# Kernel optimization log

Measured on AMD Instinct MI355X. Metric: run time of the kernel, lower is better.

Reference implementation:

```python
import jax, jax.numpy as jnp
import numpy as np

B, N, DIN, DMID, DOUT, E = 64, 5000, 64, 128, 32, 80000


def setup_inputs() -> dict:
    key = jax.random.key(0)
    ks = jax.random.split(key, 12)
    p = lambda k, shape: jax.random.normal(k, shape, jnp.float32) * 0.05
    return {
        "x": jax.random.normal(ks[0], (B, N, DIN), jnp.float32),
        "edge_index": jax.random.randint(ks[1], (2, E), 0, N),
        "prev_hidden_state": jax.random.normal(ks[2], (B, N, DMID), jnp.float32),
        # GCNConv weights/biases for gates z, r, h
        "Wg_z": p(ks[3], (DIN, DMID)), "bg_z": jnp.zeros((DMID,), jnp.float32),
        "Wg_r": p(ks[4], (DIN, DMID)), "bg_r": jnp.zeros((DMID,), jnp.float32),
        "Wg_h": p(ks[5], (DIN, DMID)), "bg_h": jnp.zeros((DMID,), jnp.float32),
        # gate Linear layers on concat([conv_out, H]) -> DMID
        "Wl_z": p(ks[6], (2 * DMID, DMID)), "bl_z": jnp.zeros((DMID,), jnp.float32),
        "Wl_r": p(ks[7], (2 * DMID, DMID)), "bl_r": jnp.zeros((DMID,), jnp.float32),
        "Wl_h": p(ks[8], (2 * DMID, DMID)), "bl_h": jnp.zeros((DMID,), jnp.float32),
        # final output Linear
        "W_out": p(ks[9], (DMID, DOUT)), "b_out": jnp.zeros((DOUT,), jnp.float32),
    }


def reference(x, edge_index, prev_hidden_state,
              Wg_z, bg_z, Wg_r, bg_r, Wg_h, bg_h,
              Wl_z, bl_z, Wl_r, bl_r, Wl_h, bl_h,
              W_out, b_out):
    # GCN symmetric normalization with self-loops (pyg gcn_norm, improved=False)
    row, col = edge_index[0], edge_index[1]
    loop = jnp.arange(N)
    src = jnp.concatenate([row, loop])          # [E+N]
    dst = jnp.concatenate([col, loop])          # [E+N]
    ew = jnp.ones((E + N,), x.dtype)
    deg = jnp.zeros((N,), x.dtype).at[dst].add(ew)
    dis = jnp.where(deg > 0, jax.lax.rsqrt(jnp.maximum(deg, 1e-12)), 0.0)
    norm = dis[src] * ew * dis[dst]             # [E+N]

    def gcn(w, b):
        xw = jnp.einsum('bnd,de->bne', x, w)            # [B,N,DMID]
        msg = xw[:, src, :] * norm[None, :, None]       # gather + weight
        out = jnp.zeros((B, N, w.shape[1]), x.dtype).at[:, dst, :].add(msg)
        return out + b

    H = prev_hidden_state
    Z = jax.nn.sigmoid(jnp.concatenate([gcn(Wg_z, bg_z), H], -1) @ Wl_z + bl_z)
    R = jax.nn.sigmoid(jnp.concatenate([gcn(Wg_r, bg_r), H], -1) @ Wl_r + bl_r)
    Ht = jnp.tanh(jnp.concatenate([gcn(Wg_h, bg_h), H * R], -1) @ Wl_h + bl_h)
    H_new = Z * H + (1.0 - Z) * Ht                      # [B,N,DMID]

    y = jnp.mean(H_new, axis=1)                         # MeanAggregation over nodes
    y = jax.nn.relu(y) @ W_out + b_out                  # [B,DOUT]
    return (y, H_new)
```

## Files before the change

### kernel.cpp

```cpp
#include <hip/hip_runtime.h>
#include <cmath>

namespace {

constexpr int B = 64, N = 5000, DIN = 64, DMID = 128, DOUT = 32, E = 80000;

typedef unsigned short u16;
typedef __attribute__((ext_vector_type(8))) short short8;
typedef __attribute__((ext_vector_type(4))) float floatx4;

#define MFMA16(a, b, c) __builtin_amdgcn_mfma_f32_16x16x32_bf16((a), (b), (c), 0, 0, 0)

__device__ __forceinline__ u16 f2bf(float f) {
  union { float f; unsigned u; } v; v.f = f;
  unsigned r = v.u + 0x7FFFu + ((v.u >> 16) & 1u);
  return (u16)(r >> 16);
}
__device__ __forceinline__ float bf2f(u16 s) {
  union { unsigned u; float f; } v; v.u = ((unsigned)s) << 16;
  return v.f;
}
__device__ __forceinline__ float sigmoid_fast(float x) {
  return __builtin_amdgcn_rcpf(1.f + __expf(-x));
}
__device__ __forceinline__ float tanh_fast(float x) {
  return fmaf(2.f, __builtin_amdgcn_rcpf(1.f + __expf(-2.f * x)), -1.f);
}


__global__ void zero_kernel(int* counts, int* fill, float* msum) {
  int i = blockIdx.x * 256 + threadIdx.x;
  if (i < N) { counts[i] = 0; fill[i] = 0; }
  if (i < B * DMID) msum[i] = 0.f;
}

__global__ void count_kernel(const int* __restrict__ ei, int* counts) {
  int e = blockIdx.x * 256 + threadIdx.x;
  if (e < E) atomicAdd(&counts[ei[E + e]], 1);
}

__global__ void scan_kernel(const int* __restrict__ counts, int* rowptr, float* dis) {
  __shared__ int sdata[1024];
  const int tid = threadIdx.x;
  constexpr int CH = (N + 1023) / 1024;
  int local[CH];
  int s = 0;
  for (int i = 0; i < CH; i++) {
    int idx = tid * CH + i;
    int c = (idx < N) ? counts[idx] : 0;
    local[i] = s;
    s += c;
  }
  sdata[tid] = s;
  __syncthreads();
  for (int off = 1; off < 1024; off <<= 1) {
    int v = (tid >= off) ? sdata[tid - off] : 0;
    __syncthreads();
    sdata[tid] += v;
    __syncthreads();
  }
  int prev = (tid > 0) ? sdata[tid - 1] : 0;
  for (int i = 0; i < CH; i++) {
    int idx = tid * CH + i;
    if (idx < N) {
      rowptr[idx] = prev + local[i];
      dis[idx] = rsqrtf((float)(counts[idx] + 1));
    }
  }
  if (tid == 1023) rowptr[N] = sdata[1023];
}

__global__ void fill_kernel(const int* __restrict__ ei, const int* __restrict__ rowptr,
                            const float* __restrict__ dis, int* fill,
                            int* csr_src, float* csr_w) {
  int e = blockIdx.x * 256 + threadIdx.x;
  if (e >= E) return;
  int r = ei[e], c = ei[E + e];
  int pos = rowptr[c] + atomicAdd(&fill[c], 1);
  csr_src[pos] = r;
  csr_w[pos] = dis[r] * dis[c];
}


__global__ void pack_kernel(const float* Wgz, const float* Wgr, const float* Wgh,
                            const float* Wlz, const float* Wlr, const float* Wlh,
                            const float* bgz, const float* bgr, const float* bgh,
                            const float* blz, const float* blr, const float* blh,
                            u16* wcB, u16* whB, float* bcAll) {
  int t = blockIdx.x * 256 + threadIdx.x;
  const float* Wg[3] = {Wgz, Wgr, Wgh};
  const float* Wl[3] = {Wlz, Wlr, Wlh};
  const float* bg[3] = {bgz, bgr, bgh};
  const float* bl[3] = {blz, blr, blh};
  if (t < 48 * 64) {
    int chunk = t >> 6, lane = t & 63;
    int q = lane >> 4, lm = lane & 15;
    int g = chunk >> 4, rem = chunk & 15, kt = rem >> 3, nt = rem & 7;
    int n = nt * 16 + lm;
#pragma unroll
    for (int jj = 0; jj < 8; jj++) {
      int k = kt * 32 + q * 8 + jj;
      float acc = 0.f;
      for (int j = 0; j < DMID; j++)
        acc = fmaf(Wg[g][k * DMID + j], Wl[g][j * DMID + n], acc);
      wcB[(size_t)(chunk * 64 + lane) * 8 + jj] = f2bf(acc);
    }
  } else if (t < 48 * 64 + 96 * 64) {
    int t2 = t - 48 * 64;
    int chunk = t2 >> 6, lane = t2 & 63;
    int q = lane >> 4, lm = lane & 15;
    int g = chunk >> 5, rem = chunk & 31, kt = rem >> 3, nt = rem & 7;
    int n = nt * 16 + lm;
#pragma unroll
    for (int jj = 0; jj < 8; jj++) {
      int k = kt * 32 + q * 8 + jj;
      whB[(size_t)t2 * 8 + jj] = f2bf(Wl[g][(DMID + k) * DMID + n]);
    }
  } else {
    int t3 = t - 48 * 64 - 96 * 64;
    if (t3 < 384) {
      int g = t3 >> 7, n = t3 & 127;
      float acc = bl[g][n];
      for (int j = 0; j < DMID; j++)
        acc = fmaf(bg[g][j], Wl[g][j * DMID + n], acc);
      bcAll[t3] = acc;
    }
  }
}


__global__ __launch_bounds__(256) void agg_kernel(
    const float* __restrict__ x, const int* __restrict__ rowptr,
    const int* __restrict__ csr_src, const float* __restrict__ csr_w,
    const float* __restrict__ dis, u16* __restrict__ xs) {
  const int sub = threadIdx.x >> 4;
  const int l16 = threadIdx.x & 15;
  const int unit = blockIdx.x * 16 + sub;
  const int b = unit / N;
  const int n = unit - b * N;
  const float* xb = x + (size_t)b * N * DIN;
  const float d = dis[n];
  float4 v = *(const float4*)(xb + (size_t)n * DIN + l16 * 4);
  const float sw = d * d;
  float ax = v.x * sw, ay = v.y * sw, az = v.z * sw, aw = v.w * sw;
  const int s1 = rowptr[n + 1];
  int p = rowptr[n];
  for (; p + 2 <= s1; p += 2) {
    int i0 = csr_src[p], i1 = csr_src[p + 1];
    float w0 = csr_w[p], w1 = csr_w[p + 1];
    float4 a0 = *(const float4*)(xb + (size_t)i0 * DIN + l16 * 4);
    float4 a1 = *(const float4*)(xb + (size_t)i1 * DIN + l16 * 4);
    ax = fmaf(a0.x, w0, ax); ay = fmaf(a0.y, w0, ay);
    az = fmaf(a0.z, w0, az); aw = fmaf(a0.w, w0, aw);
    ax = fmaf(a1.x, w1, ax); ay = fmaf(a1.y, w1, ay);
    az = fmaf(a1.z, w1, az); aw = fmaf(a1.w, w1, aw);
  }
  if (p < s1) {
    int i0 = csr_src[p];
    float w0 = csr_w[p];
    float4 a0 = *(const float4*)(xb + (size_t)i0 * DIN + l16 * 4);
    ax = fmaf(a0.x, w0, ax); ay = fmaf(a0.y, w0, ay);
    az = fmaf(a0.z, w0, az); aw = fmaf(a0.w, w0, aw);
  }
  uint2 o;
  o.x = (unsigned)f2bf(ax) | ((unsigned)f2bf(ay) << 16);
  o.y = (unsigned)f2bf(az) | ((unsigned)f2bf(aw) << 16);
  *(uint2*)(xs + (size_t)unit * DIN + l16 * 4) = o;
}


constexpr int SH = 136;
constexpr int SX = 72;

__global__ __launch_bounds__(256, 4) void fused_mfma(
    const u16* __restrict__ xs, const float* __restrict__ H,
    const u16* __restrict__ wcB, const u16* __restrict__ whB,
    const float* __restrict__ bcAll,
    float* __restrict__ hnew, float* __restrict__ msum) {
  __shared__ u16 H_s[64 * SH];
  __shared__ u16 XS_s[64 * SX];

  const int tid = threadIdx.x;
  const int b = blockIdx.y;
  const int n0 = blockIdx.x * 64;
  const int lane = tid & 63, w = tid >> 6;
  const int q = lane >> 4, lm = lane & 15;
  const int w16 = w * 16;

#pragma unroll
  for (int i = 0; i < 2; i++) {
    int idx = i * 256 + tid;
    int row = idx >> 3, seg = idx & 7;
    uint4 v = make_uint4(0u, 0u, 0u, 0u);
    if (n0 + row < N) v = *(const uint4*)(xs + ((size_t)b * N + n0 + row) * DIN + seg * 8);
    *(uint4*)&XS_s[row * SX + seg * 8] = v;
  }
#pragma unroll
  for (int i = 0; i < 8; i++) {
    int idx = i * 256 + tid;
    int row = idx >> 5, seg = idx & 31;
    float4 v = make_float4(0.f, 0.f, 0.f, 0.f);
    if (n0 + row < N) v = *(const float4*)(H + ((size_t)b * N + n0 + row) * DMID + seg * 4);
    uint2 p;
    p.x = (unsigned)f2bf(v.x) | ((unsigned)f2bf(v.y) << 16);
    p.y = (unsigned)f2bf(v.z) | ((unsigned)f2bf(v.w) << 16);
    *(uint2*)&H_s[row * SH + seg * 4] = p;
  }
  __syncthreads();

  short8 ax[2], ah[4];
#pragma unroll
  for (int kt = 0; kt < 2; kt++)
    ax[kt] = *(const short8*)&XS_s[(w16 + lm) * SX + kt * 32 + q * 8];
#pragma unroll
  for (int kt = 0; kt < 4; kt++)
    ah[kt] = *(const short8*)&H_s[(w16 + lm) * SH + kt * 32 + q * 8];

  floatx4 racc[8];
#pragma unroll
  for (int nt = 0; nt < 8; nt++) {
    floatx4 a = {0.f, 0.f, 0.f, 0.f};
#pragma unroll
    for (int kt = 0; kt < 2; kt++)
      a = MFMA16(ax[kt], *(const short8*)(wcB + (size_t)((16 + kt * 8 + nt) * 64 + lane) * 8), a);
#pragma unroll
    for (int kt = 0; kt < 4; kt++)
      a = MFMA16(ah[kt], *(const short8*)(whB + (size_t)((32 + kt * 8 + nt) * 64 + lane) * 8), a);
    float bias = bcAll[128 + nt * 16 + lm];
#pragma unroll
    for (int r = 0; r < 4; r++) racc[nt][r] = a[r] + bias;
  }

#pragma unroll
  for (int nt = 0; nt < 8; nt++)
#pragma unroll
    for (int r = 0; r < 4; r++) {
      int row = w16 + q * 4 + r, col = nt * 16 + lm;
      float h = bf2f(H_s[row * SH + col]);
      float rg = sigmoid_fast(racc[nt][r]);
      H_s[row * SH + col] = f2bf(h * rg);
      racc[nt][r] = h;
    }
  __syncthreads();

  short8 ahr[4];
#pragma unroll
  for (int kt = 0; kt < 4; kt++)
    ahr[kt] = *(const short8*)&H_s[(w16 + lm) * SH + kt * 32 + q * 8];

#pragma unroll
  for (int nt = 0; nt < 8; nt++) {
    floatx4 za = {0.f, 0.f, 0.f, 0.f}, ha = {0.f, 0.f, 0.f, 0.f};
#pragma unroll
    for (int kt = 0; kt < 2; kt++) {
      za = MFMA16(ax[kt], *(const short8*)(wcB + (size_t)((0 + kt * 8 + nt) * 64 + lane) * 8), za);
      ha = MFMA16(ax[kt], *(const short8*)(wcB + (size_t)((32 + kt * 8 + nt) * 64 + lane) * 8), ha);
    }
#pragma unroll
    for (int kt = 0; kt < 4; kt++) {
      za = MFMA16(ah[kt], *(const short8*)(whB + (size_t)((0 + kt * 8 + nt) * 64 + lane) * 8), za);
      ha = MFMA16(ahr[kt], *(const short8*)(whB + (size_t)((64 + kt * 8 + nt) * 64 + lane) * 8), ha);
    }
    float zb = bcAll[nt * 16 + lm], hb = bcAll[256 + nt * 16 + lm];
    float colsum = 0.f;
#pragma unroll
    for (int r = 0; r < 4; r++) {
      int row = w16 + q * 4 + r;
      bool valid = (n0 + row) < N;
      float z = sigmoid_fast(za[r] + zb);
      float ht = tanh_fast(ha[r] + hb);
      float h = racc[nt][r];
      float hn = fmaf(z, h - ht, ht);
      if (valid) {
        hnew[((size_t)b * N + n0 + row) * DMID + nt * 16 + lm] = hn;
        colsum += hn;
      }
    }
    colsum += __shfl_xor(colsum, 16);
    colsum += __shfl_xor(colsum, 32);
    if (lane < 16) atomicAdd(&msum[b * DMID + nt * 16 + lane], colsum);
  }
}


__global__ void out_kernel(const float* __restrict__ msum, const float* __restrict__ Wout,
                           const float* __restrict__ bout, float* __restrict__ y) {
  const int b = blockIdx.x;
  const int o = threadIdx.x;
  __shared__ float m[DMID];
  for (int jj = o; jj < DMID; jj += 32)
    m[jj] = fmaxf(msum[b * DMID + jj] * (1.f / (float)N), 0.f);
  __syncthreads();
  float acc = bout[o];
  for (int jj = 0; jj < DMID; jj++)
    acc = fmaf(m[jj], Wout[jj * DOUT + o], acc);
  y[b * DOUT + o] = acc;
}

}

extern "C" void kernel_launch(void* const* d_in, const int* in_sizes, int n_in,
                              void* d_out, int out_size, void* d_ws, size_t ws_size,
                              hipStream_t stream) {
  const float* x = (const float*)d_in[0];
  const int* ei = (const int*)d_in[1];
  const float* H = (const float*)d_in[2];
  const float* Wgz = (const float*)d_in[3];
  const float* bgz = (const float*)d_in[4];
  const float* Wgr = (const float*)d_in[5];
  const float* bgr = (const float*)d_in[6];
  const float* Wgh = (const float*)d_in[7];
  const float* bgh = (const float*)d_in[8];
  const float* Wlz = (const float*)d_in[9];
  const float* blz = (const float*)d_in[10];
  const float* Wlr = (const float*)d_in[11];
  const float* blr = (const float*)d_in[12];
  const float* Wlh = (const float*)d_in[13];
  const float* blh = (const float*)d_in[14];
  const float* Wout = (const float*)d_in[15];
  const float* bout = (const float*)d_in[16];

  float* y = (float*)d_out;
  float* hnew = (float*)d_out + (size_t)B * DOUT;

  char* p = (char*)d_ws;
  auto carve = [&](size_t bytes) {
    char* q = p;
    p += (bytes + 255) & ~size_t(255);
    return q;
  };
  int* counts = (int*)carve((size_t)N * 4);
  int* rowptr = (int*)carve((size_t)(N + 1) * 4);
  int* fill = (int*)carve((size_t)N * 4);
  int* csr_src = (int*)carve((size_t)E * 4);
  float* csr_w = (float*)carve((size_t)E * 4);
  float* dis = (float*)carve((size_t)N * 4);
  float* msum = (float*)carve((size_t)B * DMID * 4);
  u16* wcB = (u16*)carve((size_t)48 * 64 * 8 * 2);
  u16* whB = (u16*)carve((size_t)96 * 64 * 8 * 2);
  float* bcAll = (float*)carve((size_t)384 * 4);
  u16* xs = (u16*)carve((size_t)B * N * DIN * 2);

  zero_kernel<<<(B * DMID + 255) / 256, 256, 0, stream>>>(counts, fill, msum);
  pack_kernel<<<38, 256, 0, stream>>>(Wgz, Wgr, Wgh, Wlz, Wlr, Wlh,
                                      bgz, bgr, bgh, blz, blr, blh,
                                      wcB, whB, bcAll);
  count_kernel<<<(E + 255) / 256, 256, 0, stream>>>(ei, counts);
  scan_kernel<<<1, 1024, 0, stream>>>(counts, rowptr, dis);
  fill_kernel<<<(E + 255) / 256, 256, 0, stream>>>(ei, rowptr, dis, fill, csr_src, csr_w);
  agg_kernel<<<B * N / 16, 256, 0, stream>>>(x, rowptr, csr_src, csr_w, dis, xs);
  fused_mfma<<<dim3((N + 63) / 64, B), 256, 0, stream>>>(xs, H, wcB, whB, bcAll,
                                                         hnew, msum);
  out_kernel<<<B, 32, 0, stream>>>(msum, Wout, bout, y);
}
```

Before: 702.5 us.

## Replace global mean atomics with per-block partials, remap agg blocks, raise occupancy

The fused kernel now accumulates column sums into shared memory and writes one partial row per block. The output kernel reduces those partials, so global float atomics and the msum zeroing are no longer needed. The aggregation kernel permutes block indices across 8 strided groups, apparently to spread blocks over XCDs for better cache locality. The fused kernel's launch bounds rise from 4 to 6 blocks per CU, which may force register spills.

```diff
diff --git a/kernel.cpp b/kernel.cpp
--- a/kernel.cpp
+++ b/kernel.cpp
@@ -4,6 +4,7 @@
 namespace {
 
 constexpr int B = 64, N = 5000, DIN = 64, DMID = 128, DOUT = 32, E = 80000;
+constexpr int NT = (N + 63) / 64;
 
 typedef unsigned short u16;
 typedef __attribute__((ext_vector_type(8))) short short8;
@@ -28,10 +29,9 @@
 }
 
 
-__global__ void zero_kernel(int* counts, int* fill, float* msum) {
+__global__ void zero_kernel(int* counts, int* fill) {
   int i = blockIdx.x * 256 + threadIdx.x;
   if (i < N) { counts[i] = 0; fill[i] = 0; }
-  if (i < B * DMID) msum[i] = 0.f;
 }
 
 __global__ void count_kernel(const int* __restrict__ ei, int* counts) {
@@ -133,9 +133,12 @@
     const float* __restrict__ x, const int* __restrict__ rowptr,
     const int* __restrict__ csr_src, const float* __restrict__ csr_w,
     const float* __restrict__ dis, u16* __restrict__ xs) {
+  constexpr int G = B * N / 16;
+  const int bid = blockIdx.x;
+  const int nb = (bid & 7) * (G >> 3) + (bid >> 3);
   const int sub = threadIdx.x >> 4;
   const int l16 = threadIdx.x & 15;
-  const int unit = blockIdx.x * 16 + sub;
+  const int unit = nb * 16 + sub;
   const int b = unit / N;
   const int n = unit - b * N;
   const float* xb = x + (size_t)b * N * DIN;
@@ -172,13 +175,14 @@
 constexpr int SH = 136;
 constexpr int SX = 72;
 
-__global__ __launch_bounds__(256, 4) void fused_mfma(
+__global__ __launch_bounds__(256, 6) void fused_mfma(
     const u16* __restrict__ xs, const float* __restrict__ H,
     const u16* __restrict__ wcB, const u16* __restrict__ whB,
     const float* __restrict__ bcAll,
-    float* __restrict__ hnew, float* __restrict__ msum) {
+    float* __restrict__ hnew, float* __restrict__ partials) {
   __shared__ u16 H_s[64 * SH];
   __shared__ u16 XS_s[64 * SX];
+  __shared__ float lds_sum[DMID];
 
   const int tid = threadIdx.x;
   const int b = blockIdx.y;
@@ -186,6 +190,8 @@
   const int lane = tid & 63, w = tid >> 6;
   const int q = lane >> 4, lm = lane & 15;
   const int w16 = w * 16;
+
+  if (tid < DMID) lds_sum[tid] = 0.f;
 
 #pragma unroll
   for (int i = 0; i < 2; i++) {
@@ -278,23 +284,31 @@
     }
     colsum += __shfl_xor(colsum, 16);
     colsum += __shfl_xor(colsum, 32);
-    if (lane < 16) atomicAdd(&msum[b * DMID + nt * 16 + lane], colsum);
-  }
-}
-
-
-__global__ void out_kernel(const float* __restrict__ msum, const float* __restrict__ Wout,
+    if (lane < 16) atomicAdd(&lds_sum[nt * 16 + lane], colsum);
+  }
+
+  __syncthreads();
+  if (tid < DMID)
+    partials[((size_t)b * NT + blockIdx.x) * DMID + tid] = lds_sum[tid];
+}
+
+
+__global__ void out_kernel(const float* __restrict__ partials, const float* __restrict__ Wout,
                            const float* __restrict__ bout, float* __restrict__ y) {
   const int b = blockIdx.x;
-  const int o = threadIdx.x;
+  const int c = threadIdx.x;
   __shared__ float m[DMID];
-  for (int jj = o; jj < DMID; jj += 32)
-    m[jj] = fmaxf(msum[b * DMID + jj] * (1.f / (float)N), 0.f);
-  __syncthreads();
-  float acc = bout[o];
-  for (int jj = 0; jj < DMID; jj++)
-    acc = fmaf(m[jj], Wout[jj * DOUT + o], acc);
-  y[b * DOUT + o] = acc;
+  float acc = 0.f;
+  for (int t = 0; t < NT; t++)
+    acc += partials[((size_t)b * NT + t) * DMID + c];
+  m[c] = fmaxf(acc * (1.f / (float)N), 0.f);
+  __syncthreads();
+  if (c < DOUT) {
+    float a2 = bout[c];
+    for (int jj = 0; jj < DMID; jj++)
+      a2 = fmaf(m[jj], Wout[jj * DOUT + c], a2);
+    y[b * DOUT + c] = a2;
+  }
 }
 
 }
@@ -335,13 +349,13 @@
   int* csr_src = (int*)carve((size_t)E * 4);
   float* csr_w = (float*)carve((size_t)E * 4);
   float* dis = (float*)carve((size_t)N * 4);
-  float* msum = (float*)carve((size_t)B * DMID * 4);
   u16* wcB = (u16*)carve((size_t)48 * 64 * 8 * 2);
   u16* whB = (u16*)carve((size_t)96 * 64 * 8 * 2);
   float* bcAll = (float*)carve((size_t)384 * 4);
+  float* partials = (float*)carve((size_t)B * NT * DMID * 4);
   u16* xs = (u16*)carve((size_t)B * N * DIN * 2);
 
-  zero_kernel<<<(B * DMID + 255) / 256, 256, 0, stream>>>(counts, fill, msum);
+  zero_kernel<<<(N + 255) / 256, 256, 0, stream>>>(counts, fill);
   pack_kernel<<<38, 256, 0, stream>>>(Wgz, Wgr, Wgh, Wlz, Wlr, Wlh,
                                       bgz, bgr, bgh, blz, blr, blh,
                                       wcB, whB, bcAll);
@@ -349,7 +363,6 @@
   scan_kernel<<<1, 1024, 0, stream>>>(counts, rowptr, dis);
   fill_kernel<<<(E + 255) / 256, 256, 0, stream>>>(ei, rowptr, dis, fill, csr_src, csr_w);
   agg_kernel<<<B * N / 16, 256, 0, stream>>>(x, rowptr, csr_src, csr_w, dis, xs);
-  fused_mfma<<<dim3((N + 63) / 64, B), 256, 0, stream>>>(xs, H, wcB, whB, bcAll,
-                                                         hnew, msum);
-  out_kernel<<<B, 32, 0, stream>>>(msum, Wout, bout, y);
-}
+  fused_mfma<<<dim3(NT, B), 256, 0, stream>>>(xs, H, wcB, whB, bcAll, hnew, partials);
+  out_kernel<<<B, DMID, 0, stream>>>(partials, Wout, bout, y);
+}
```

Result: slower. 854.7 us (+21.7%).
